# Optimization experiments

Measured on AMD Instinct MI355X. Metric: run time of the kernel, lower is better.

## Reference

```python
import jax, jax.numpy as jnp
import numpy as np
from math import sqrt

D_MODEL = 1024
NUM_HEADS = 16
MASK_VAL = -100000000.0


def setup_inputs() -> dict:
    key = jax.random.key(0)
    k1, k2, k3, k4, k5 = jax.random.split(key, 5)
    scale = 1.0 / sqrt(D_MODEL)
    return {
        "in_features": jax.random.normal(k1, (2, 2048, D_MODEL), dtype=jnp.float32),
        "q_proj_weight": jax.random.normal(k2, (D_MODEL, D_MODEL), dtype=jnp.float32) * scale,
        "k_proj_weight": jax.random.normal(k3, (D_MODEL, D_MODEL), dtype=jnp.float32) * scale,
        "v_proj_weight": jax.random.normal(k4, (D_MODEL, D_MODEL), dtype=jnp.float32) * scale,
        "o_proj_weight": jax.random.normal(k5, (D_MODEL, D_MODEL), dtype=jnp.float32) * scale,
    }


def _proj_heads(x, w, h):
    # x: [b, s, d_in], w: [h*d, d_in] -> [b, h, s, d]
    d = w.shape[0] // h
    w = w.reshape(h, d, w.shape[1])
    return jnp.einsum('bsi,hdi->bhsd', x, w)


def reference(in_features, q_proj_weight, k_proj_weight, v_proj_weight, o_proj_weight):
    h = NUM_HEADS
    b, s, _ = in_features.shape
    q = _proj_heads(in_features, q_proj_weight, h)  # [b,h,s,dk]
    k = _proj_heads(in_features, k_proj_weight, h)
    v = _proj_heads(in_features, v_proj_weight, h)
    d_k = q.shape[-1]
    # additive causal mask: -1e8 above diagonal
    mask = jnp.triu(jnp.full((s, s), MASK_VAL, dtype=q.dtype), k=1)[None, None]
    scores = jnp.einsum('bhqd,bhkd->bhqk', q, k) / sqrt(d_k) + mask
    attn = jax.nn.softmax(scores, axis=-1)
    out = jnp.einsum('bhqk,bhkd->bhqd', attn, v)          # [b,h,s,dv]
    out = out.transpose(0, 2, 1, 3).reshape(b, s, -1)      # [b,s,h*dv]
    return jnp.einsum('bsv,mv->bsm', out, o_proj_weight)
```

## Files before the change

kernel.cpp:

```cpp
#include <hip/hip_runtime.h>
#include <hip/hip_bf16.h>
#include <stdint.h>
#include <type_traits>

typedef __bf16 bf16;
typedef __bf16 bf16x4 __attribute__((ext_vector_type(4)));
typedef __bf16 bf16x8 __attribute__((ext_vector_type(8)));
typedef float floatx4 __attribute__((ext_vector_type(4)));
typedef unsigned int u32;

#define D_MODEL 1024
#define SEQ 2048
#define NHEADS 16
#define DH 64
#define BATCH 2
#define MROWS (BATCH * SEQ)

#define XELEMS ((size_t)MROWS * D_MODEL)
#define WELEMS ((size_t)D_MODEL * D_MODEL)
#define CVT_ELEMS (XELEMS + 4 * WELEMS)

__device__ __forceinline__ void gload_lds16(const void* g, void* l) {
  __builtin_amdgcn_global_load_lds(
      (const __attribute__((address_space(1))) u32*)g,
      (__attribute__((address_space(3))) u32*)l, 16, 0, 0);
}

__global__ __launch_bounds__(256) void cvt_f32_bf16(
    const float* __restrict__ s0, const float* __restrict__ s1,
    const float* __restrict__ s2, const float* __restrict__ s3,
    const float* __restrict__ s4, bf16* __restrict__ dst) {
  const size_t i = ((size_t)blockIdx.x * 256 + threadIdx.x) * 8;
  const float* src;
  size_t off;
  if (i < XELEMS) {
    src = s0; off = i;
  } else {
    const size_t j = i - XELEMS;
    const int r = (int)(j / WELEMS);
    src = (r == 0) ? s1 : (r == 1) ? s2 : (r == 2) ? s3 : s4;
    off = j - (size_t)r * WELEMS;
  }
  floatx4 f0 = *(const floatx4*)&src[off];
  floatx4 f1 = *(const floatx4*)&src[off + 4];
  bf16x8 o;
#pragma unroll
  for (int j = 0; j < 4; j++) { o[j] = (bf16)f0[j]; o[4 + j] = (bf16)f1[j]; }
  *(bf16x8*)&dst[i] = o;
}


__global__ __launch_bounds__(256) void gemm_qkv(
    const bf16* __restrict__ A, const bf16* __restrict__ Wq,
    const bf16* __restrict__ Wk, const bf16* __restrict__ Wv,
    bf16* __restrict__ Qo, bf16* __restrict__ Ko, bf16* __restrict__ Vto) {
  const int z = blockIdx.z;
  const bf16* W = (z == 0) ? Wq : (z == 1) ? Wk : Wv;

  __shared__ bf16 As[128 * 64];
  __shared__ bf16 Bs[128 * 64];

  const int tid = threadIdx.x;
  const int lane = tid & 63;
  const int w = tid >> 6;
  const int lo16 = lane & 15;
  const int quad = lane >> 4;
  const int wy = w >> 1, wx = w & 1;

  const int m0 = blockIdx.y * 128;
  const int n0 = blockIdx.x * 128;

  const int sl = lane >> 3;
  const int sc = ((lane & 7) ^ sl) * 8;

  const floatx4 fz = {0.f, 0.f, 0.f, 0.f};
  floatx4 acc[4][4];
#pragma unroll
  for (int i = 0; i < 4; i++)
#pragma unroll
    for (int j = 0; j < 4; j++) acc[i][j] = fz;

  auto kloop = [&](auto vt) {
    constexpr bool VT = decltype(vt)::value;
    for (int k0 = 0; k0 < 1024; k0 += 64) {
      __syncthreads();
#pragma unroll
      for (int i = 0; i < 4; i++) {
        const int seg = i * 4 + w;
        const int row = seg * 8 + sl;
        gload_lds16(&A[(size_t)(m0 + row) * 1024 + k0 + sc], &As[seg * 512]);
        gload_lds16(&W[(size_t)(n0 + row) * 1024 + k0 + sc], &Bs[seg * 512]);
      }
      __syncthreads();

#pragma unroll
      for (int kk = 0; kk < 64; kk += 32) {
        bf16x8 af[4], bfr[4];
        const int cc = (kk >> 3) + quad;
#pragma unroll
        for (int t = 0; t < 4; t++) {
          const int ra = wy * 64 + t * 16 + lo16;
          const int rb = wx * 64 + t * 16 + lo16;
          af[t]  = *(const bf16x8*)&As[ra * 64 + ((cc ^ (ra & 7)) << 3)];
          bfr[t] = *(const bf16x8*)&Bs[rb * 64 + ((cc ^ (rb & 7)) << 3)];
        }
#pragma unroll
        for (int mt = 0; mt < 4; mt++)
#pragma unroll
          for (int nt = 0; nt < 4; nt++) {
            if constexpr (VT)
              acc[mt][nt] = __builtin_amdgcn_mfma_f32_16x16x32_bf16(bfr[nt], af[mt], acc[mt][nt], 0, 0, 0);
            else
              acc[mt][nt] = __builtin_amdgcn_mfma_f32_16x16x32_bf16(af[mt], bfr[nt], acc[mt][nt], 0, 0, 0);
          }
      }
    }
  };
  if (z == 2) kloop(std::true_type{}); else kloop(std::false_type{});

  if (z < 2) {
    bf16* C = (z == 0) ? Qo : Ko;
#pragma unroll
    for (int mt = 0; mt < 4; mt++)
#pragma unroll
      for (int nt = 0; nt < 4; nt++)
#pragma unroll
        for (int r = 0; r < 4; r++) {
          const int row = m0 + wy * 64 + mt * 16 + quad * 4 + r;
          const int col = n0 + wx * 64 + nt * 16 + lo16;
          C[(size_t)row * D_MODEL + col] = (bf16)acc[mt][nt][r];
        }
  } else {
#pragma unroll
    for (int mt = 0; mt < 4; mt++)
#pragma unroll
      for (int nt = 0; nt < 4; nt++)
#pragma unroll
        for (int r = 0; r < 4; r++) {
          const int feat = n0 + wx * 64 + nt * 16 + quad * 4 + r;
          const int tok  = m0 + wy * 64 + mt * 16 + lo16;
          const int hh = feat >> 6, dd = feat & 63;
          const int bb = tok >> 11, ss = tok & 2047;
          Vto[(size_t)((bb * NHEADS + hh) * DH + dd) * SEQ + ss] = (bf16)acc[mt][nt][r];
        }
  }
}

__global__ __launch_bounds__(256) void gemm_o(
    const bf16* __restrict__ A, const bf16* __restrict__ W,
    float* __restrict__ C) {
  __shared__ bf16 As[64 * 64];
  __shared__ bf16 Bs[128 * 64];

  const int tid = threadIdx.x;
  const int lane = tid & 63;
  const int w = tid >> 6;
  const int lo16 = lane & 15;
  const int quad = lane >> 4;
  const int wy = w >> 1, wx = w & 1;

  const int m0 = blockIdx.y * 64;
  const int n0 = blockIdx.x * 128;

  const int sl = lane >> 3;
  const int sc = ((lane & 7) ^ sl) * 8;

  const floatx4 fz = {0.f, 0.f, 0.f, 0.f};
  floatx4 acc[2][4];
#pragma unroll
  for (int i = 0; i < 2; i++)
#pragma unroll
    for (int j = 0; j < 4; j++) acc[i][j] = fz;

  for (int k0 = 0; k0 < 1024; k0 += 64) {
    __syncthreads();
#pragma unroll
    for (int i = 0; i < 2; i++) {
      const int seg = i * 4 + w;
      const int row = seg * 8 + sl;
      gload_lds16(&A[(size_t)(m0 + row) * 1024 + k0 + sc], &As[seg * 512]);
    }
#pragma unroll
    for (int i = 0; i < 4; i++) {
      const int seg = i * 4 + w;
      const int row = seg * 8 + sl;
      gload_lds16(&W[(size_t)(n0 + row) * 1024 + k0 + sc], &Bs[seg * 512]);
    }
    __syncthreads();

#pragma unroll
    for (int kk = 0; kk < 64; kk += 32) {
      const int cc = (kk >> 3) + quad;
      bf16x8 af[2], bfr[4];
#pragma unroll
      for (int t = 0; t < 2; t++) {
        const int ra = wy * 32 + t * 16 + lo16;
        af[t] = *(const bf16x8*)&As[ra * 64 + ((cc ^ (ra & 7)) << 3)];
      }
#pragma unroll
      for (int t = 0; t < 4; t++) {
        const int rb = wx * 64 + t * 16 + lo16;
        bfr[t] = *(const bf16x8*)&Bs[rb * 64 + ((cc ^ (rb & 7)) << 3)];
      }
#pragma unroll
      for (int mt = 0; mt < 2; mt++)
#pragma unroll
        for (int nt = 0; nt < 4; nt++)
          acc[mt][nt] = __builtin_amdgcn_mfma_f32_16x16x32_bf16(af[mt], bfr[nt], acc[mt][nt], 0, 0, 0);
    }
  }

#pragma unroll
  for (int mt = 0; mt < 2; mt++)
#pragma unroll
    for (int nt = 0; nt < 4; nt++)
#pragma unroll
      for (int r = 0; r < 4; r++) {
        const int row = m0 + wy * 32 + mt * 16 + quad * 4 + r;
        const int col = n0 + wx * 64 + nt * 16 + lo16;
        C[(size_t)row * D_MODEL + col] = acc[mt][nt][r];
      }
}

#define LP 72

__global__ __launch_bounds__(256) void attn_causal(
    const bf16* __restrict__ Q, const bf16* __restrict__ Kg,
    const bf16* __restrict__ Vt, bf16* __restrict__ O) {
  __shared__ bf16 Ks[64 * LP];
  __shared__ bf16 VTs[64 * LP];
  __shared__ bf16 Ps[4][16 * LP];

  const int tid = threadIdx.x;
  const int lane = tid & 63;
  const int w = tid >> 6;
  const int lo16 = lane & 15;
  const int quad = lane >> 4;

  const int x = blockIdx.x;
  const int qtA = x;
  const int qtB = 31 - x;
  const int tmax = qtB;
  const int h = blockIdx.y;
  const int b = blockIdx.z;
  const size_t base  = (size_t)b * SEQ * D_MODEL + (size_t)h * DH;
  const size_t baset = (size_t)(b * NHEADS + h) * DH * SEQ;

  const int rA = qtA * 64 + w * 16 + lo16;
  const int rB = qtB * 64 + w * 16 + lo16;
  bf16x8 qfA[2], qfB[2];
#pragma unroll
  for (int ks = 0; ks < 2; ks++) {
    qfA[ks] = *(const bf16x8*)&Q[base + (size_t)rA * D_MODEL + ks * 32 + quad * 8];
    qfB[ks] = *(const bf16x8*)&Q[base + (size_t)rB * D_MODEL + ks * 32 + quad * 8];
  }

  const floatx4 fz = {0.f, 0.f, 0.f, 0.f};
  floatx4 oA[4], oB[4];
  float lA = 0.f, lB = 0.f;
#pragma unroll
  for (int i = 0; i < 4; i++) { oA[i] = fz; oB[i] = fz; }

  const int kr = tid >> 3;
  const int kc = (tid & 7) * 8;

  bf16x8 kv[2], vv[2];
#pragma unroll
  for (int c = 0; c < 2; c++) {
    kv[c] = *(const bf16x8*)&Kg[base + (size_t)(c * 32 + kr) * D_MODEL + kc];
    vv[c] = *(const bf16x8*)&Vt[baset + (size_t)(c * 32 + kr) * SEQ + kc];
  }

  for (int t = 0; t <= tmax; t++) {
    const int j0 = t * 64;
    __syncthreads();
#pragma unroll
    for (int c = 0; c < 2; c++) {
      *(bf16x8*)&Ks[(c * 32 + kr) * LP + kc] = kv[c];
      *(bf16x8*)&VTs[(c * 32 + kr) * LP + kc] = vv[c];
    }
    __syncthreads();

    if (t < tmax) {
      const int j1 = j0 + 64;
#pragma unroll
      for (int c = 0; c < 2; c++) {
        kv[c] = *(const bf16x8*)&Kg[base + (size_t)(j1 + c * 32 + kr) * D_MODEL + kc];
        vv[c] = *(const bf16x8*)&Vt[baset + (size_t)(c * 32 + kr) * SEQ + j1 + kc];
      }
    }

    bf16x8 kf[4][2], vf[2][4];
#pragma unroll
    for (int nt = 0; nt < 4; nt++)
#pragma unroll
      for (int ks = 0; ks < 2; ks++)
        kf[nt][ks] = *(const bf16x8*)&Ks[(nt * 16 + lo16) * LP + ks * 32 + quad * 8];
#pragma unroll
    for (int ks = 0; ks < 2; ks++)
#pragma unroll
      for (int dt = 0; dt < 4; dt++)
        vf[ks][dt] = *(const bf16x8*)&VTs[(dt * 16 + lo16) * LP + ks * 32 + quad * 8];

    auto compute = [&](int q0s, const bf16x8* qf, floatx4* oacc, float& lsum,
                       bool diag) {
      floatx4 sacc[4];
#pragma unroll
      for (int nt = 0; nt < 4; nt++) sacc[nt] = fz;
#pragma unroll
      for (int nt = 0; nt < 4; nt++)
#pragma unroll
        for (int ks = 0; ks < 2; ks++)
          sacc[nt] = __builtin_amdgcn_mfma_f32_16x16x32_bf16(kf[nt][ks], qf[ks], sacc[nt], 0, 0, 0);

      const int myq = q0s + w * 16 + lo16;
#pragma unroll
      for (int nt = 0; nt < 4; nt++) {
        const int kvb = j0 + nt * 16 + quad * 4;
        float p[4];
#pragma unroll
        for (int r = 0; r < 4; r++) {
          const float e = __builtin_amdgcn_exp2f(fmaf(sacc[nt][r], 0.18033688f, -17.3123405f));
          p[r] = (diag && (kvb + r > myq)) ? 0.f : e;
          lsum += p[r];
        }
        bf16x4 pk;
#pragma unroll
        for (int r = 0; r < 4; r++) pk[r] = (bf16)p[r];
        *(bf16x4*)&Ps[w][lo16 * LP + nt * 16 + quad * 4] = pk;
      }

#pragma unroll
      for (int ks = 0; ks < 2; ks++) {
        bf16x8 pf = *(const bf16x8*)&Ps[w][lo16 * LP + ks * 32 + quad * 8];
#pragma unroll
        for (int dt = 0; dt < 4; dt++)
          oacc[dt] = __builtin_amdgcn_mfma_f32_16x16x32_bf16(pf, vf[ks][dt], oacc[dt], 0, 0, 0);
      }
    };

    compute(qtB * 64, qfB, oB, lB, t == qtB);
    if (t <= qtA) compute(qtA * 64, qfA, oA, lA, t == qtA);
  }

  auto finish = [&](int q0s, floatx4* oacc, float lsum) {
    lsum += __shfl_xor(lsum, 16);
    lsum += __shfl_xor(lsum, 32);
#pragma unroll
    for (int r = 0; r < 4; r++) {
      const float lr = __shfl(lsum, quad * 4 + r);
      const float inv = 1.0f / lr;
      const int row = q0s + w * 16 + quad * 4 + r;
#pragma unroll
      for (int dt = 0; dt < 4; dt++)
        O[base + (size_t)row * D_MODEL + dt * 16 + lo16] = (bf16)(oacc[dt][r] * inv);
    }
  };
  finish(qtA * 64, oA, lA);
  finish(qtB * 64, oB, lB);
}

extern "C" void kernel_launch(void* const* d_in, const int* in_sizes, int n_in,
                              void* d_out, int out_size, void* d_ws, size_t ws_size,
                              hipStream_t stream) {
  const float* X  = (const float*)d_in[0];
  const float* Wq = (const float*)d_in[1];
  const float* Wk = (const float*)d_in[2];
  const float* Wv = (const float*)d_in[3];
  const float* Wo = (const float*)d_in[4];
  float* out = (float*)d_out;

  bf16* cvt = (bf16*)d_ws;
  bf16* Xb  = cvt;
  bf16* Wqb = cvt + XELEMS;
  bf16* Wkb = Wqb + WELEMS;
  bf16* Wvb = Wkb + WELEMS;
  bf16* Wob = Wvb + WELEMS;
  bf16* Qb  = cvt + CVT_ELEMS;
  bf16* Kb  = Qb + XELEMS;
  bf16* Vtb = Kb + XELEMS;
  bf16* Ob  = Vtb + XELEMS;

  dim3 blk(256);
  cvt_f32_bf16<<<dim3((u32)(CVT_ELEMS / (256 * 8))), blk, 0, stream>>>(
      X, Wq, Wk, Wv, Wo, cvt);
  gemm_qkv<<<dim3(8, 32, 3), blk, 0, stream>>>(Xb, Wqb, Wkb, Wvb, Qb, Kb, Vtb);
  attn_causal<<<dim3(16, NHEADS, BATCH), blk, 0, stream>>>(Qb, Kb, Vtb, Ob);
  gemm_o<<<dim3(8, 64), blk, 0, stream>>>(Ob, Wob, out);
}
```

Baseline: 181.5 us.

## Compute softmax row sums via MFMA with ones, split diag path, deepen O-proj K tile

In the attention kernel, the per-lane scalar row-sum accumulation and cross-lane shuffles are replaced by an extra MFMA that multiplies the bf16 probability tile by a ones vector, so the denominator lands in the same layout as the output accumulator. The exp/mask loop is also split into separate diagonal and off-diagonal branches so off-diagonal tiles skip the mask compare. The output-projection GEMM now loads a 128-wide K slab per barrier pair, halving the number of synchronizations, at the cost of doubled LDS use. Summing bf16-rounded probabilities changes numerics slightly, which makes the denominator consistent with the numerator.

```diff
diff --git a/kernel.cpp b/kernel.cpp
--- a/kernel.cpp
+++ b/kernel.cpp
@@ -149,8 +149,8 @@
 __global__ __launch_bounds__(256) void gemm_o(
     const bf16* __restrict__ A, const bf16* __restrict__ W,
     float* __restrict__ C) {
-  __shared__ bf16 As[64 * 64];
-  __shared__ bf16 Bs[128 * 64];
+  __shared__ bf16 As[2 * 64 * 64];
+  __shared__ bf16 Bs[2 * 128 * 64];
 
   const int tid = threadIdx.x;
   const int lane = tid & 63;
@@ -172,35 +172,41 @@
 #pragma unroll
     for (int j = 0; j < 4; j++) acc[i][j] = fz;
 
-  for (int k0 = 0; k0 < 1024; k0 += 64) {
+  for (int k0 = 0; k0 < 1024; k0 += 128) {
     __syncthreads();
 #pragma unroll
-    for (int i = 0; i < 2; i++) {
-      const int seg = i * 4 + w;
-      const int row = seg * 8 + sl;
-      gload_lds16(&A[(size_t)(m0 + row) * 1024 + k0 + sc], &As[seg * 512]);
-    }
-#pragma unroll
-    for (int i = 0; i < 4; i++) {
-      const int seg = i * 4 + w;
-      const int row = seg * 8 + sl;
-      gload_lds16(&W[(size_t)(n0 + row) * 1024 + k0 + sc], &Bs[seg * 512]);
+    for (int kh = 0; kh < 2; kh++) {
+#pragma unroll
+      for (int i = 0; i < 2; i++) {
+        const int seg = i * 4 + w;
+        const int row = seg * 8 + sl;
+        gload_lds16(&A[(size_t)(m0 + row) * 1024 + k0 + kh * 64 + sc],
+                    &As[kh * 4096 + seg * 512]);
+      }
+#pragma unroll
+      for (int i = 0; i < 4; i++) {
+        const int seg = i * 4 + w;
+        const int row = seg * 8 + sl;
+        gload_lds16(&W[(size_t)(n0 + row) * 1024 + k0 + kh * 64 + sc],
+                    &Bs[kh * 8192 + seg * 512]);
+      }
     }
     __syncthreads();
 
 #pragma unroll
-    for (int kk = 0; kk < 64; kk += 32) {
-      const int cc = (kk >> 3) + quad;
+    for (int kk = 0; kk < 128; kk += 32) {
+      const int kh = kk >> 6;
+      const int cc = ((kk & 63) >> 3) + quad;
       bf16x8 af[2], bfr[4];
 #pragma unroll
       for (int t = 0; t < 2; t++) {
         const int ra = wy * 32 + t * 16 + lo16;
-        af[t] = *(const bf16x8*)&As[ra * 64 + ((cc ^ (ra & 7)) << 3)];
+        af[t] = *(const bf16x8*)&As[kh * 4096 + ra * 64 + ((cc ^ (ra & 7)) << 3)];
       }
 #pragma unroll
       for (int t = 0; t < 4; t++) {
         const int rb = wx * 64 + t * 16 + lo16;
-        bfr[t] = *(const bf16x8*)&Bs[rb * 64 + ((cc ^ (rb & 7)) << 3)];
+        bfr[t] = *(const bf16x8*)&Bs[kh * 8192 + rb * 64 + ((cc ^ (rb & 7)) << 3)];
       }
 #pragma unroll
       for (int mt = 0; mt < 2; mt++)
@@ -255,9 +261,13 @@
     qfB[ks] = *(const bf16x8*)&Q[base + (size_t)rB * D_MODEL + ks * 32 + quad * 8];
   }
 
+  bf16x8 onesf;
+#pragma unroll
+  for (int j = 0; j < 8; j++) onesf[j] = (bf16)1.0f;
+
   const floatx4 fz = {0.f, 0.f, 0.f, 0.f};
   floatx4 oA[4], oB[4];
-  float lA = 0.f, lB = 0.f;
+  floatx4 lA = fz, lB = fz;
 #pragma unroll
   for (int i = 0; i < 4; i++) { oA[i] = fz; oB[i] = fz; }
 
@@ -302,7 +312,7 @@
       for (int dt = 0; dt < 4; dt++)
         vf[ks][dt] = *(const bf16x8*)&VTs[(dt * 16 + lo16) * LP + ks * 32 + quad * 8];
 
-    auto compute = [&](int q0s, const bf16x8* qf, floatx4* oacc, float& lsum,
+    auto compute = [&](int q0s, const bf16x8* qf, floatx4* oacc, floatx4& lacc,
                        bool diag) {
       floatx4 sacc[4];
 #pragma unroll
@@ -313,21 +323,28 @@
         for (int ks = 0; ks < 2; ks++)
           sacc[nt] = __builtin_amdgcn_mfma_f32_16x16x32_bf16(kf[nt][ks], qf[ks], sacc[nt], 0, 0, 0);
 
-      const int myq = q0s + w * 16 + lo16;
-#pragma unroll
-      for (int nt = 0; nt < 4; nt++) {
-        const int kvb = j0 + nt * 16 + quad * 4;
-        float p[4];
-#pragma unroll
-        for (int r = 0; r < 4; r++) {
-          const float e = __builtin_amdgcn_exp2f(fmaf(sacc[nt][r], 0.18033688f, -17.3123405f));
-          p[r] = (diag && (kvb + r > myq)) ? 0.f : e;
-          lsum += p[r];
+      if (diag) {
+        const int myq = q0s + w * 16 + lo16;
+#pragma unroll
+        for (int nt = 0; nt < 4; nt++) {
+          const int kvb = j0 + nt * 16 + quad * 4;
+          bf16x4 pk;
+#pragma unroll
+          for (int r = 0; r < 4; r++) {
+            const float e = __builtin_amdgcn_exp2f(fmaf(sacc[nt][r], 0.18033688f, -17.3123405f));
+            pk[r] = (bf16)((kvb + r > myq) ? 0.f : e);
+          }
+          *(bf16x4*)&Ps[w][lo16 * LP + nt * 16 + quad * 4] = pk;
         }
-        bf16x4 pk;
-#pragma unroll
-        for (int r = 0; r < 4; r++) pk[r] = (bf16)p[r];
-        *(bf16x4*)&Ps[w][lo16 * LP + nt * 16 + quad * 4] = pk;
+      } else {
+#pragma unroll
+        for (int nt = 0; nt < 4; nt++) {
+          bf16x4 pk;
+#pragma unroll
+          for (int r = 0; r < 4; r++)
+            pk[r] = (bf16)__builtin_amdgcn_exp2f(fmaf(sacc[nt][r], 0.18033688f, -17.3123405f));
+          *(bf16x4*)&Ps[w][lo16 * LP + nt * 16 + quad * 4] = pk;
+        }
       }
 
 #pragma unroll
@@ -336,6 +353,7 @@
 #pragma unroll
         for (int dt = 0; dt < 4; dt++)
           oacc[dt] = __builtin_amdgcn_mfma_f32_16x16x32_bf16(pf, vf[ks][dt], oacc[dt], 0, 0, 0);
+        lacc = __builtin_amdgcn_mfma_f32_16x16x32_bf16(pf, onesf, lacc, 0, 0, 0);
       }
     };
 
@@ -343,13 +361,10 @@
     if (t <= qtA) compute(qtA * 64, qfA, oA, lA, t == qtA);
   }
 
-  auto finish = [&](int q0s, floatx4* oacc, float lsum) {
-    lsum += __shfl_xor(lsum, 16);
-    lsum += __shfl_xor(lsum, 32);
+  auto finish = [&](int q0s, floatx4* oacc, floatx4 lacc) {
 #pragma unroll
     for (int r = 0; r < 4; r++) {
-      const float lr = __shfl(lsum, quad * 4 + r);
-      const float inv = 1.0f / lr;
+      const float inv = 1.0f / lacc[r];
       const int row = q0s + w * 16 + quad * 4 + r;
 #pragma unroll
       for (int dt = 0; dt < 4; dt++)
```

After: 180.9 us. About the same (-0.3%).
